# Kernel tuning notes

Measured on AMD Instinct MI355X. Metric: run time of the kernel, lower is better.

Reference implementation:

```python
import jax, jax.numpy as jnp
import numpy as np
from math import sqrt

SCALE = sqrt(512.0)  # max(key_size, attn_hidden_size, query_size) with scaled=True

def setup_inputs() -> dict:
    key = jax.random.key(0)
    k1, k2, k3, k4, k5 = jax.random.split(key, 5)
    B, T, S, M, N, H = 8, 512, 512, 512, 512, 128
    return {
        "query": jax.random.normal(k1, (B, T, M), dtype=jnp.float32),
        "keys": jax.random.normal(k2, (B, S, N), dtype=jnp.float32),
        "W1": jax.random.normal(k3, (N, H), dtype=jnp.float32),
        "W2": jax.random.normal(k4, (M, H), dtype=jnp.float32),
        "v": jax.random.normal(k5, (H,), dtype=jnp.float32),
    }

def reference(query, keys, W1, W2, v):
    # Project query and keys into attention hidden space
    x1 = jnp.einsum('btm,mh->bth', query, W2)   # (B,T,H)
    x2 = jnp.einsum('bsn,nh->bsh', keys, W1)    # (B,S,H)
    # Broadcast merge (op='add'), tanh activation, v-weighted reduction over H
    merged = jnp.tanh(x1[:, :, None, :] + x2[:, None, :, :])  # (B,T,S,H)
    score = jnp.einsum('btsh,h->bts', merged, v)
    return score / SCALE
```

## Files before the change

kernel.cpp:

```cpp
#include <hip/hip_runtime.h>
#include <hip/hip_fp16.h>


constexpr float SCALE_IN  = 2.8853900817779268f;
constexpr float INV_SCALE = 0.04419417382415922f;

typedef float v2f __attribute__((ext_vector_type(2)));

__device__ __forceinline__ v2f exp2v(v2f z) {
  v2f r;
  r.x = __builtin_amdgcn_exp2f(z.x);
  r.y = __builtin_amdgcn_exp2f(z.y);
  return r;
}
__device__ __forceinline__ v2f rcpv(v2f d) {
  v2f r;
  r.x = __builtin_amdgcn_rcpf(d.x);
  r.y = __builtin_amdgcn_rcpf(d.y);
  return r;
}

__global__ __launch_bounds__(512) void proj_kernel(
    const float* __restrict__ q,  const float* __restrict__ w2,
    const float* __restrict__ ky, const float* __restrict__ w1,
    float* __restrict__ x1z, float* __restrict__ x2z) {
  __shared__ float As[32 * 64];
  __shared__ float Ws[64 * 128];

  int blk = blockIdx.x;
  const float* A; const float* W; float* O;
  if (blk < 128) { A = q;  W = w2; O = x1z; }
  else           { blk -= 128; A = ky; W = w1; O = x2z; }
  const int rbase = blk * 32;
  const int tid = threadIdx.x;

  const int rq = tid >> 5;
  const int hq = tid & 31;

  float acc[2][4];
#pragma unroll
  for (int r = 0; r < 2; ++r)
#pragma unroll
    for (int c = 0; c < 4; ++c) acc[r][c] = 0.0f;

  for (int kb = 0; kb < 512; kb += 64) {
    {
      const int arow = tid >> 4;
      const int kq4  = (tid & 15) * 4;
      *(float4*)(As + arow * 64 + kq4) =
          *(const float4*)(A + (size_t)(rbase + arow) * 512 + kb + kq4);
      const int wrow = tid >> 5;
      const int hq4  = (tid & 31) * 4;
#pragma unroll
      for (int p = 0; p < 4; ++p)
        *(float4*)(Ws + (wrow + 16 * p) * 128 + hq4) =
            *(const float4*)(W + (size_t)(kb + wrow + 16 * p) * 128 + hq4);
    }
    __syncthreads();
#pragma unroll 4
    for (int k4 = 0; k4 < 64; k4 += 4) {
      float a[2][4], w[4][4];
      *(float4*)a[0] = *(const float4*)(As + (2 * rq + 0) * 64 + k4);
      *(float4*)a[1] = *(const float4*)(As + (2 * rq + 1) * 64 + k4);
#pragma unroll
      for (int kk = 0; kk < 4; ++kk)
        *(float4*)w[kk] = *(const float4*)(Ws + (k4 + kk) * 128 + 4 * hq);
#pragma unroll
      for (int kk = 0; kk < 4; ++kk)
#pragma unroll
        for (int r = 0; r < 2; ++r)
#pragma unroll
          for (int c = 0; c < 4; ++c)
            acc[r][c] = fmaf(a[r][kk], w[kk][c], acc[r][c]);
    }
    __syncthreads();
  }

#pragma unroll
  for (int r = 0; r < 2; ++r) {
    float4 z;
    z.x = acc[r][0] * SCALE_IN;
    z.y = acc[r][1] * SCALE_IN;
    z.z = acc[r][2] * SCALE_IN;
    z.w = acc[r][3] * SCALE_IN;
    *(float4*)(O + (size_t)(rbase + 2 * rq + r) * 128 + 4 * hq) = z;
  }
}

__global__ __launch_bounds__(512, 4) void score_kernel(
    const float* __restrict__ x1z, const float* __restrict__ x2z,
    const float* __restrict__ v, float* __restrict__ out) {
  __shared__ float x1l[64 * 64];
  __shared__ float x2l[64 * 64];

  const int tid   = threadIdx.x;
  const int b     = blockIdx.x >> 6;
  const int tile  = blockIdx.x & 63;
  const int tbase = (tile >> 3) * 64;
  const int sbase = (tile & 7) * 64;

  const float* x1g = x1z + (size_t)(b * 512 + tbase) * 128;
  const float* x2g = x2z + (size_t)(b * 512 + sbase) * 128;

  const int sg = tid & 15;
  const int tg = tid >> 4;

  v2f racc[2][2];
#pragma unroll
  for (int i = 0; i < 2; ++i)
#pragma unroll
    for (int jp = 0; jp < 2; ++jp) racc[i][jp] = (v2f){0.0f, 0.0f};
  float sv = 0.0f;

  const v2f C30 = {30.0f, 30.0f};

  for (int ph = 0; ph < 2; ++ph) {
    {
      const int r1 = tid & 63;
      const int c0 = tid >> 6;
#pragma unroll
      for (int p = 0; p < 2; ++p) {
        const int c = c0 + 8 * p;
        const float4 a =
            *(const float4*)(x1g + (size_t)r1 * 128 + ph * 64 + 4 * c);
        x1l[(4 * c + 0) * 64 + r1] = a.x;
        x1l[(4 * c + 1) * 64 + r1] = a.y;
        x1l[(4 * c + 2) * 64 + r1] = a.z;
        x1l[(4 * c + 3) * 64 + r1] = a.w;
        const float4 s =
            *(const float4*)(x2g + (size_t)r1 * 128 + ph * 64 + 4 * c);
        x2l[(4 * c + 0) * 64 + r1] = s.x;
        x2l[(4 * c + 1) * 64 + r1] = s.y;
        x2l[(4 * c + 2) * 64 + r1] = s.z;
        x2l[(4 * c + 3) * 64 + r1] = s.w;
      }
    }
    __syncthreads();

    for (int hg = 0; hg < 16; ++hg) {
      const int h0 = hg * 4;
      const float4 vq = *(const float4*)(v + ph * 64 + h0);
      sv += (vq.x + vq.y) + (vq.z + vq.w);

      float zt[2][4];
      v2f   zs[2][4];
#pragma unroll
      for (int qq = 0; qq < 4; ++qq) {
        const float2 tp = *(const float2*)(x1l + (h0 + qq) * 64 + 2 * tg);
        zt[0][qq] = tp.x;
        zt[1][qq] = tp.y;
        const float4 sp = *(const float4*)(x2l + (h0 + qq) * 64 + 4 * sg);
        zs[0][qq] = (v2f){sp.x, sp.y};
        zs[1][qq] = (v2f){sp.z, sp.w};
      }

#pragma unroll
      for (int i = 0; i < 2; ++i) {
#pragma unroll
        for (int jp = 0; jp < 2; ++jp) {
          const v2f e0 =
              exp2v(__builtin_elementwise_min(zt[i][0] + zs[jp][0], C30));
          const v2f e1 =
              exp2v(__builtin_elementwise_min(zt[i][1] + zs[jp][1], C30));
          const v2f e2 =
              exp2v(__builtin_elementwise_min(zt[i][2] + zs[jp][2], C30));
          const v2f e3 =
              exp2v(__builtin_elementwise_min(zt[i][3] + zs[jp][3], C30));
          const v2f A0 = e0 + 1.0f, A1 = e1 + 1.0f;
          const v2f A2 = e2 + 1.0f, A3 = e3 + 1.0f;
          const v2f P12 = A0 * A1, P34 = A2 * A3;
          const v2f U1 = vq.x * A1 + vq.y * A0;
          const v2f U2 = vq.z * A3 + vq.w * A2;
          const v2f NUM = U1 * P34 + U2 * P12;
          const v2f DEN = P12 * P34;
          racc[i][jp] += NUM * rcpv(DEN);
        }
      }
    }
    __syncthreads();
  }

  const float c1v = sv * INV_SCALE;
  const float c2v = -2.0f * INV_SCALE;
#pragma unroll
  for (int i = 0; i < 2; ++i) {
    const int t = tbase + 2 * tg + i;
    float4 o;
    o.x = fmaf(racc[i][0].x, c2v, c1v);
    o.y = fmaf(racc[i][0].y, c2v, c1v);
    o.z = fmaf(racc[i][1].x, c2v, c1v);
    o.w = fmaf(racc[i][1].y, c2v, c1v);
    *(float4*)(out + (size_t)(b * 512 + t) * 512 + sbase + 4 * sg) = o;
  }
}

extern "C" void kernel_launch(void* const* d_in, const int* in_sizes, int n_in,
                              void* d_out, int out_size, void* d_ws, size_t ws_size,
                              hipStream_t stream) {
  const float* query = (const float*)d_in[0];
  const float* keys  = (const float*)d_in[1];
  const float* W1    = (const float*)d_in[2];
  const float* W2    = (const float*)d_in[3];
  const float* v     = (const float*)d_in[4];
  float* out = (float*)d_out;

  float* x1zp = (float*)d_ws;
  float* x2zp = x1zp + 8 * 512 * 128;

  hipLaunchKernelGGL(proj_kernel, dim3(256), dim3(512), 0, stream,
                     query, W2, keys, W1, x1zp, x2zp);
  hipLaunchKernelGGL(score_kernel, dim3(512), dim3(512), 0, stream,
                     x1zp, x2zp, v, out);
}
```

Before: 140.3 us.

## Batch eight tanh terms per reciprocal and register-prefetch projection tiles

The score kernel now combines eight v-weighted sigmoid terms over one common denominator instead of four. That halves the reciprocal count per h element and cuts some multiply work, but it lowers the exp2 clamp to 14 so the product of eight factors stays within float range, which may affect accuracy. The projection kernel also prefetches the next A/W tile into registers while computing the current one, to hide global load latency.

```diff
diff --git a/kernel.cpp b/kernel.cpp
--- a/kernel.cpp
+++ b/kernel.cpp
@@ -43,20 +43,35 @@
 #pragma unroll
     for (int c = 0; c < 4; ++c) acc[r][c] = 0.0f;
 
+  const int arow = tid >> 4;
+  const int kq4  = (tid & 15) * 4;
+  const int wrow = tid >> 5;
+  const int wg   = (tid & 31) * 4;
+
+  const float* Abase = A + (size_t)(rbase + arow) * 512 + kq4;
+  const float* Wbase = W + (size_t)wrow * 128 + wg;
+
+  float4 areg = *(const float4*)(Abase);
+  float4 wreg[4];
+#pragma unroll
+  for (int p = 0; p < 4; ++p)
+    wreg[p] = *(const float4*)(Wbase + (size_t)(16 * p) * 128);
+
   for (int kb = 0; kb < 512; kb += 64) {
-    {
-      const int arow = tid >> 4;
-      const int kq4  = (tid & 15) * 4;
-      *(float4*)(As + arow * 64 + kq4) =
-          *(const float4*)(A + (size_t)(rbase + arow) * 512 + kb + kq4);
-      const int wrow = tid >> 5;
-      const int hq4  = (tid & 31) * 4;
+    *(float4*)(As + arow * 64 + kq4) = areg;
+#pragma unroll
+    for (int p = 0; p < 4; ++p)
+      *(float4*)(Ws + (wrow + 16 * p) * 128 + wg) = wreg[p];
+    __syncthreads();
+
+    if (kb < 448) {
+      areg = *(const float4*)(Abase + kb + 64);
 #pragma unroll
       for (int p = 0; p < 4; ++p)
-        *(float4*)(Ws + (wrow + 16 * p) * 128 + hq4) =
-            *(const float4*)(W + (size_t)(kb + wrow + 16 * p) * 128 + hq4);
-    }
-    __syncthreads();
+        wreg[p] =
+            *(const float4*)(Wbase + (size_t)(kb + 64 + 16 * p) * 128);
+    }
+
 #pragma unroll 4
     for (int k4 = 0; k4 < 64; k4 += 4) {
       float a[2][4], w[4][4];
@@ -112,7 +127,7 @@
     for (int jp = 0; jp < 2; ++jp) racc[i][jp] = (v2f){0.0f, 0.0f};
   float sv = 0.0f;
 
-  const v2f C30 = {30.0f, 30.0f};
+  const v2f C14 = {14.0f, 14.0f};
 
   for (int ph = 0; ph < 2; ++ph) {
     {
@@ -137,15 +152,17 @@
     }
     __syncthreads();
 
-    for (int hg = 0; hg < 16; ++hg) {
-      const int h0 = hg * 4;
-      const float4 vq = *(const float4*)(v + ph * 64 + h0);
-      sv += (vq.x + vq.y) + (vq.z + vq.w);
-
-      float zt[2][4];
-      v2f   zs[2][4];
-#pragma unroll
-      for (int qq = 0; qq < 4; ++qq) {
+    for (int hg = 0; hg < 8; ++hg) {
+      const int h0 = hg * 8;
+      const float4 vq0 = *(const float4*)(v + ph * 64 + h0);
+      const float4 vq1 = *(const float4*)(v + ph * 64 + h0 + 4);
+      sv += (vq0.x + vq0.y) + (vq0.z + vq0.w) +
+            (vq1.x + vq1.y) + (vq1.z + vq1.w);
+
+      float zt[2][8];
+      v2f   zs[2][8];
+#pragma unroll
+      for (int qq = 0; qq < 8; ++qq) {
         const float2 tp = *(const float2*)(x1l + (h0 + qq) * 64 + 2 * tg);
         zt[0][qq] = tp.x;
         zt[1][qq] = tp.y;
@@ -158,22 +175,25 @@
       for (int i = 0; i < 2; ++i) {
 #pragma unroll
         for (int jp = 0; jp < 2; ++jp) {
-          const v2f e0 =
-              exp2v(__builtin_elementwise_min(zt[i][0] + zs[jp][0], C30));
-          const v2f e1 =
-              exp2v(__builtin_elementwise_min(zt[i][1] + zs[jp][1], C30));
-          const v2f e2 =
-              exp2v(__builtin_elementwise_min(zt[i][2] + zs[jp][2], C30));
-          const v2f e3 =
-              exp2v(__builtin_elementwise_min(zt[i][3] + zs[jp][3], C30));
-          const v2f A0 = e0 + 1.0f, A1 = e1 + 1.0f;
-          const v2f A2 = e2 + 1.0f, A3 = e3 + 1.0f;
-          const v2f P12 = A0 * A1, P34 = A2 * A3;
-          const v2f U1 = vq.x * A1 + vq.y * A0;
-          const v2f U2 = vq.z * A3 + vq.w * A2;
-          const v2f NUM = U1 * P34 + U2 * P12;
-          const v2f DEN = P12 * P34;
-          racc[i][jp] += NUM * rcpv(DEN);
+          v2f A[8];
+#pragma unroll
+          for (int qq = 0; qq < 8; ++qq) {
+            const v2f e =
+                exp2v(__builtin_elementwise_min(zt[i][qq] + zs[jp][qq], C14));
+            A[qq] = e + 1.0f;
+          }
+          const v2f P01 = A[0] * A[1], P23 = A[2] * A[3];
+          const v2f P45 = A[4] * A[5], P67 = A[6] * A[7];
+          const v2f P0123 = P01 * P23, P4567 = P45 * P67;
+          const v2f D = P0123 * P4567;
+          const v2f u01 = vq0.x * A[1] + vq0.y * A[0];
+          const v2f u23 = vq0.z * A[3] + vq0.w * A[2];
+          const v2f u45 = vq1.x * A[5] + vq1.y * A[4];
+          const v2f u67 = vq1.z * A[7] + vq1.w * A[6];
+          const v2f n0123 = u01 * P23 + u23 * P01;
+          const v2f n4567 = u45 * P67 + u67 * P45;
+          const v2f NUM = n0123 * P4567 + n4567 * P0123;
+          racc[i][jp] += NUM * rcpv(D);
         }
       }
     }
```

Result: slower. 152.4 us (+8.6%).
